# Performance work log

Measured on AMD Instinct MI355X. Metric: run time of the kernel, lower is better.

The kernel has to match this reference:

```python
import jax, jax.numpy as jnp
import numpy as np

EPS = 1e-8
TOPK = 10


def setup_inputs() -> dict:
    key = jax.random.key(0)
    kz, ky = jax.random.split(key)
    B, C, T = 128, 512, 512
    Z = jax.random.normal(kz, (B, C, T), dtype=jnp.float32)
    Y = jax.random.normal(ky, (B, C, T), dtype=jnp.float32)
    return {"Z": Z, "Y": Y}


def reference(Z, Y):
    B = Z.shape[0]
    x = Z.reshape(B, -1)  # [B, D]
    y = Y.reshape(B, -1)  # [B, D]
    # cosine similarity: sim[i, j] = x[i] . y[j] / max(|x[i]| * |y[j]|, eps)
    dots = jnp.einsum("id,jd->ij", x, y)  # [B, B]
    xn = jnp.linalg.norm(x, axis=1)  # [B]
    yn = jnp.linalg.norm(y, axis=1)  # [B]
    sim = dots / jnp.maximum(xn[:, None] * yn[None, :], EPS)
    sim = sim.T  # rows now indexed by Y, cols by Z (as in original)
    diags = jnp.arange(B)
    top1accuracy = jnp.mean((jnp.argmax(sim, axis=1) == diags).astype(jnp.float32))
    _, topk_idx = jax.lax.top_k(sim, TOPK)  # [B, 10]
    top10accuracy = jnp.mean(jnp.any(topk_idx == diags[:, None], axis=1).astype(jnp.float32))
    return (top1accuracy, top10accuracy)
```

## Files before the change

### kernel.cpp

```cpp
#include <hip/hip_runtime.h>
#include <hip/hip_bf16.h>
#include <math.h>


#define DIMD 262144

typedef short  bf16x8  __attribute__((ext_vector_type(8)));
typedef float  floatx4 __attribute__((ext_vector_type(4)));

union FragU { uint4 u; bf16x8 v; };

__global__ __launch_bounds__(512, 4)
void mfma_dot_kernel(const float* __restrict__ Z, const float* __restrict__ Y,
                     float* __restrict__ partials, float* __restrict__ norms,
                     int NT) {
    __shared__ __align__(16) ushort planes[4][128][40];

    const int tid = threadIdx.x;
    const int lid = tid & 63;
    const int w   = tid >> 6;

    const int srow = tid >> 3;
    const int q    = tid & 7;

    const int m0 = 64 * (w >> 2);
    const int n0 = 32 * (w & 3);
    const int fr = lid & 15;
    const int fk = (lid >> 4) * 8;

    floatx4 acc[4][2];
#pragma unroll
    for (int a = 0; a < 4; ++a)
#pragma unroll
        for (int b = 0; b < 2; ++b)
            acc[a][b] = (floatx4){0.f, 0.f, 0.f, 0.f};

    float z2[2] = {0.f, 0.f}, y2[2] = {0.f, 0.f};

    const uint kbase = (uint)blockIdx.x * (uint)(NT * 32);
    const uint off0  = (uint)srow * (uint)DIMD + kbase + 4u * (uint)q;
    const uint off1  = off0 + 64u * (uint)DIMD;

    float4 za[2], ya[2], zb[2], yb[2];
    za[0] = *(const float4*)(Z + off0);      za[1] = *(const float4*)(Z + off1);
    ya[0] = *(const float4*)(Y + off0);      ya[1] = *(const float4*)(Y + off1);
    zb[0] = *(const float4*)(Z + off0 + 32); zb[1] = *(const float4*)(Z + off1 + 32);
    yb[0] = *(const float4*)(Y + off0 + 32); yb[1] = *(const float4*)(Y + off1 + 32);

    auto convstore = [&](const float4 (&zr)[2], const float4 (&yr)[2]) {
#pragma unroll
        for (int i = 0; i < 2; ++i) {
            const int row = srow + 64 * i;
            {
                const float4 v = zr[i];
                const uint h0 = __float_as_uint(v.x) >> 16, h1 = __float_as_uint(v.y) >> 16;
                const uint h2 = __float_as_uint(v.z) >> 16, h3 = __float_as_uint(v.w) >> 16;
                const uint l0 = __float_as_uint(v.x - __uint_as_float(h0 << 16)) >> 16;
                const uint l1 = __float_as_uint(v.y - __uint_as_float(h1 << 16)) >> 16;
                const uint l2 = __float_as_uint(v.z - __uint_as_float(h2 << 16)) >> 16;
                const uint l3 = __float_as_uint(v.w - __uint_as_float(h3 << 16)) >> 16;
                *(uint2*)&planes[0][row][4 * q] =
                    make_uint2(h0 | (h1 << 16), h2 | (h3 << 16));
                *(uint2*)&planes[1][row][4 * q] =
                    make_uint2(l0 | (l1 << 16), l2 | (l3 << 16));
                z2[i] += v.x * v.x + v.y * v.y + v.z * v.z + v.w * v.w;
            }
            {
                const float4 v = yr[i];
                const uint h0 = __float_as_uint(v.x) >> 16, h1 = __float_as_uint(v.y) >> 16;
                const uint h2 = __float_as_uint(v.z) >> 16, h3 = __float_as_uint(v.w) >> 16;
                const uint l0 = __float_as_uint(v.x - __uint_as_float(h0 << 16)) >> 16;
                const uint l1 = __float_as_uint(v.y - __uint_as_float(h1 << 16)) >> 16;
                const uint l2 = __float_as_uint(v.z - __uint_as_float(h2 << 16)) >> 16;
                const uint l3 = __float_as_uint(v.w - __uint_as_float(h3 << 16)) >> 16;
                *(uint2*)&planes[2][row][4 * q] =
                    make_uint2(h0 | (h1 << 16), h2 | (h3 << 16));
                *(uint2*)&planes[3][row][4 * q] =
                    make_uint2(l0 | (l1 << 16), l2 | (l3 << 16));
                y2[i] += v.x * v.x + v.y * v.y + v.z * v.z + v.w * v.w;
            }
        }
    };

    auto mfma_phase = [&]() {
        FragU bh[2], bl[2];
#pragma unroll
        for (int tn = 0; tn < 2; ++tn) {
            bh[tn].u = *(const uint4*)&planes[2][n0 + 16 * tn + fr][fk];
            bl[tn].u = *(const uint4*)&planes[3][n0 + 16 * tn + fr][fk];
        }
#pragma unroll
        for (int tm = 0; tm < 4; ++tm) {
            FragU ah, al;
            ah.u = *(const uint4*)&planes[0][m0 + 16 * tm + fr][fk];
            al.u = *(const uint4*)&planes[1][m0 + 16 * tm + fr][fk];
#pragma unroll
            for (int tn = 0; tn < 2; ++tn) {
                acc[tm][tn] = __builtin_amdgcn_mfma_f32_16x16x32_bf16(ah.v, bh[tn].v, acc[tm][tn], 0, 0, 0);
                acc[tm][tn] = __builtin_amdgcn_mfma_f32_16x16x32_bf16(ah.v, bl[tn].v, acc[tm][tn], 0, 0, 0);
                acc[tm][tn] = __builtin_amdgcn_mfma_f32_16x16x32_bf16(al.v, bh[tn].v, acc[tm][tn], 0, 0, 0);
            }
        }
    };

#pragma unroll 1
    for (int t = 0; t < NT; t += 2) {
        __syncthreads();
        convstore(za, ya);
        if (t + 2 < NT) {
            const uint ko = (uint)(t + 2) * 32u;
            za[0] = *(const float4*)(Z + off0 + ko); za[1] = *(const float4*)(Z + off1 + ko);
            ya[0] = *(const float4*)(Y + off0 + ko); ya[1] = *(const float4*)(Y + off1 + ko);
        }
        __syncthreads();
        mfma_phase();

        __syncthreads();
        convstore(zb, yb);
        if (t + 3 < NT) {
            const uint ko = (uint)(t + 3) * 32u;
            zb[0] = *(const float4*)(Z + off0 + ko); zb[1] = *(const float4*)(Z + off1 + ko);
            yb[0] = *(const float4*)(Y + off0 + ko); yb[1] = *(const float4*)(Y + off1 + ko);
        }
        __syncthreads();
        mfma_phase();
    }

#pragma unroll
    for (int m = 1; m <= 4; m <<= 1) {
        z2[0] += __shfl_xor(z2[0], m); z2[1] += __shfl_xor(z2[1], m);
        y2[0] += __shfl_xor(y2[0], m); y2[1] += __shfl_xor(y2[1], m);
    }
    if (q == 0) {
        atomicAdd(&norms[srow],            z2[0]);
        atomicAdd(&norms[srow + 64],       z2[1]);
        atomicAdd(&norms[128 + srow],      y2[0]);
        atomicAdd(&norms[128 + srow + 64], y2[1]);
    }

    float* P = partials + (size_t)blockIdx.x * 16384;
    const int rq = (lid >> 4) * 4;
#pragma unroll
    for (int tm = 0; tm < 4; ++tm)
#pragma unroll
        for (int tn = 0; tn < 2; ++tn)
#pragma unroll
            for (int r = 0; r < 4; ++r)
                P[(size_t)(m0 + 16 * tm + rq + r) * 128 + (n0 + 16 * tn + fr)] =
                    acc[tm][tn][r];
}

#define BK   16
#define LSTR 132
__global__ __launch_bounds__(256)
void dot_norm_atomic(const float* __restrict__ Z, const float* __restrict__ Y,
                     float* __restrict__ dots, float* __restrict__ norms,
                     int KC) {
    __shared__ float lA[BK][LSTR];
    __shared__ float lB[BK][LSTR];
    const int tid = threadIdx.x;
    const int tx = tid & 15, ty = tid >> 4;
    const int r0 = ty * 8, c0 = tx * 8;
    const int rowm = tid >> 2, kq = tid & 3;
    float acc[8][8];
#pragma unroll
    for (int i = 0; i < 8; ++i)
#pragma unroll
        for (int j = 0; j < 8; ++j) acc[i][j] = 0.f;
    float a2s0 = 0.f, a2s1 = 0.f, b2s0 = 0.f, b2s1 = 0.f;
    const size_t kbase = (size_t)blockIdx.x * KC;
    const size_t offA0 = (size_t)rowm * DIMD + kbase + kq * 4;
    const size_t offA1 = (size_t)(rowm + 64) * DIMD + kbase + kq * 4;
    const int niter = KC / BK;
#pragma unroll 1
    for (int t = 0; t < niter; ++t) {
        const size_t ko = (size_t)t * BK;
        const float4 av0 = *(const float4*)(Z + offA0 + ko);
        const float4 av1 = *(const float4*)(Z + offA1 + ko);
        const float4 bv0 = *(const float4*)(Y + offA0 + ko);
        const float4 bv1 = *(const float4*)(Y + offA1 + ko);
        a2s0 += av0.x*av0.x + av0.y*av0.y + av0.z*av0.z + av0.w*av0.w;
        a2s1 += av1.x*av1.x + av1.y*av1.y + av1.z*av1.z + av1.w*av1.w;
        b2s0 += bv0.x*bv0.x + bv0.y*bv0.y + bv0.z*bv0.z + bv0.w*bv0.w;
        b2s1 += bv1.x*bv1.x + bv1.y*bv1.y + bv1.z*bv1.z + bv1.w*bv1.w;
        __syncthreads();
        const int kk = kq * 4;
        lA[kk+0][rowm]    = av0.x; lA[kk+1][rowm]    = av0.y;
        lA[kk+2][rowm]    = av0.z; lA[kk+3][rowm]    = av0.w;
        lA[kk+0][rowm+64] = av1.x; lA[kk+1][rowm+64] = av1.y;
        lA[kk+2][rowm+64] = av1.z; lA[kk+3][rowm+64] = av1.w;
        lB[kk+0][rowm]    = bv0.x; lB[kk+1][rowm]    = bv0.y;
        lB[kk+2][rowm]    = bv0.z; lB[kk+3][rowm]    = bv0.w;
        lB[kk+0][rowm+64] = bv1.x; lB[kk+1][rowm+64] = bv1.y;
        lB[kk+2][rowm+64] = bv1.z; lB[kk+3][rowm+64] = bv1.w;
        __syncthreads();
#pragma unroll
        for (int k = 0; k < BK; ++k) {
            const float4 a0 = *(const float4*)&lA[k][r0];
            const float4 a1 = *(const float4*)&lA[k][r0 + 4];
            const float4 b0 = *(const float4*)&lB[k][c0];
            const float4 b1 = *(const float4*)&lB[k][c0 + 4];
            const float a[8] = {a0.x,a0.y,a0.z,a0.w,a1.x,a1.y,a1.z,a1.w};
            const float b[8] = {b0.x,b0.y,b0.z,b0.w,b1.x,b1.y,b1.z,b1.w};
#pragma unroll
            for (int i = 0; i < 8; ++i)
#pragma unroll
                for (int j = 0; j < 8; ++j)
                    acc[i][j] = fmaf(a[i], b[j], acc[i][j]);
        }
    }
    __syncthreads();
    float* nrm = &lA[0][0];
    nrm[tid] = 0.f;
    __syncthreads();
    atomicAdd(&nrm[rowm],            a2s0);
    atomicAdd(&nrm[rowm + 64],       a2s1);
    atomicAdd(&nrm[128 + rowm],      b2s0);
    atomicAdd(&nrm[128 + rowm + 64], b2s1);
    __syncthreads();
    atomicAdd(&norms[tid], nrm[tid]);
#pragma unroll
    for (int i = 0; i < 8; ++i)
#pragma unroll
        for (int j = 0; j < 8; ++j)
            atomicAdd(&dots[(size_t)(r0 + i) * 128 + (c0 + j)], acc[i][j]);
}

__global__ __launch_bounds__(256)
void reduce_stage1(const float* __restrict__ partials, float* __restrict__ stage,
                   int per_chunk) {
    const int g = blockIdx.x * 256 + threadIdx.x;
    const int f4 = g & 4095;
    const int chunk = g >> 12;
    const float4* p = (const float4*)partials;
    float4 s = make_float4(0.f, 0.f, 0.f, 0.f);
    const size_t base = (size_t)chunk * per_chunk;
    for (int k = 0; k < per_chunk; ++k) {
        const float4 v = p[(base + k) * 4096 + f4];
        s.x += v.x; s.y += v.y; s.z += v.z; s.w += v.w;
    }
    ((float4*)stage)[(size_t)chunk * 4096 + f4] = s;
}

__global__ __launch_bounds__(128)
void rank_kernel(const float* __restrict__ stage, const float* __restrict__ norms,
                 float* __restrict__ out, int nchunks) {
    __shared__ float sim[128];
    __shared__ int cnt;
    const int a = blockIdx.x;
    const int b = threadIdx.x;
    float s = 0.f;
    for (int c = 0; c < nchunks; ++c)
        s += stage[(size_t)c * 16384 + (size_t)b * 128 + a];
    const float v = s / fmaxf(sqrtf(norms[b]) * sqrtf(norms[128 + a]), 1e-8f);
    sim[b] = v;
    if (b == 0) cnt = 0;
    __syncthreads();
    const float diag = sim[a];
    if (b != a && v > diag) atomicAdd(&cnt, 1);
    __syncthreads();
    if (b == 0) {
        if (cnt == 0) atomicAdd(&out[0], 1.0f / 128.0f);
        if (cnt < 10) atomicAdd(&out[1], 1.0f / 128.0f);
    }
}

extern "C" void kernel_launch(void* const* d_in, const int* in_sizes, int n_in,
                              void* d_out, int out_size, void* d_ws, size_t ws_size,
                              hipStream_t stream) {
    const float* Z = (const float*)d_in[0];
    const float* Y = (const float*)d_in[1];
    float* dots     = (float*)d_ws;
    float* norms    = dots + 128 * 128;
    float* stage    = norms + 256;
    float* partials = stage + 32 * 16384;
    float* out      = (float*)d_out;

    const size_t head_floats = 128 * 128 + 256 + 32 * 16384;
    int nb = 0;
    const int cands[2] = {512, 256};
    for (int c = 0; c < 2; ++c) {
        if ((head_floats + (size_t)cands[c] * 16384) * sizeof(float) <= ws_size) {
            nb = cands[c];
            break;
        }
    }

    hipMemsetAsync(d_ws, 0, (128 * 128 + 256) * sizeof(float), stream);
    hipMemsetAsync(d_out, 0, 2 * sizeof(float), stream);

    if (nb > 0) {
        mfma_dot_kernel<<<nb, 512, 0, stream>>>(Z, Y, partials, norms,
                                                DIMD / nb / 32);
        reduce_stage1<<<512, 256, 0, stream>>>(partials, stage, nb / 32);
        rank_kernel<<<128, 128, 0, stream>>>(stage, norms, out, 32);
    } else {
        dot_norm_atomic<<<512, 256, 0, stream>>>(Z, Y, dots, norms, DIMD / 512);
        rank_kernel<<<128, 128, 0, stream>>>(dots, norms, out, 1);
    }
}
```

Baseline: 317.9 us.

## Stage fp32 tiles via direct global-to-LDS loads, convert to bf16 hi/lo at fragment load

Replaces register-staged loads plus conversion and store into bf16 planes with asynchronous global_load_lds copies of raw fp32 tiles into a double-buffered, XOR-swizzled LDS layout. The hi/lo bf16 split now happens per fragment when reading from LDS, and the squared norms are computed from the LDS tile. This removes one barrier per step and the VGPR round-trip, letting the next tile load overlap the MFMA work. The cost is doubled LDS footprint, which may lower occupancy, and redundant conversion work, since each fragment row is converted by several waves.

```diff
diff --git a/kernel.cpp b/kernel.cpp
--- a/kernel.cpp
+++ b/kernel.cpp
@@ -9,24 +9,47 @@
 typedef float  floatx4 __attribute__((ext_vector_type(4)));
 
 union FragU { uint4 u; bf16x8 v; };
+
+#define GLOAD_LDS16(g, l)                                        \
+    __builtin_amdgcn_global_load_lds(                            \
+        (const __attribute__((address_space(1))) void*)(g),      \
+        (__attribute__((address_space(3))) void*)(l), 16, 0, 0)
+
+static __device__ __forceinline__ void cvt_hilo(const float4 f0, const float4 f1,
+                                                bf16x8& hv, bf16x8& lv) {
+    const float ff[8] = {f0.x, f0.y, f0.z, f0.w, f1.x, f1.y, f1.z, f1.w};
+    uint hu[4], lu[4];
+#pragma unroll
+    for (int j = 0; j < 4; ++j) {
+        const uint b0  = __float_as_uint(ff[2 * j]);
+        const uint b1  = __float_as_uint(ff[2 * j + 1]);
+        const uint hf0 = b0 & 0xffff0000u;
+        const uint hf1 = b1 & 0xffff0000u;
+        hu[j] = (b0 >> 16) | hf1;
+        const uint lo0 = __float_as_uint(ff[2 * j]     - __uint_as_float(hf0));
+        const uint lo1 = __float_as_uint(ff[2 * j + 1] - __uint_as_float(hf1));
+        lu[j] = (lo0 >> 16) | (lo1 & 0xffff0000u);
+    }
+    FragU h, l;
+    h.u = make_uint4(hu[0], hu[1], hu[2], hu[3]);
+    l.u = make_uint4(lu[0], lu[1], lu[2], lu[3]);
+    hv = h.v; lv = l.v;
+}
 
 __global__ __launch_bounds__(512, 4)
 void mfma_dot_kernel(const float* __restrict__ Z, const float* __restrict__ Y,
                      float* __restrict__ partials, float* __restrict__ norms,
                      int NT) {
-    __shared__ __align__(16) ushort planes[4][128][40];
+    __shared__ __align__(16) float ldsf[2][2][128][32];
 
     const int tid = threadIdx.x;
     const int lid = tid & 63;
     const int w   = tid >> 6;
 
-    const int srow = tid >> 3;
-    const int q    = tid & 7;
-
-    const int m0 = 64 * (w >> 2);
-    const int n0 = 32 * (w & 3);
-    const int fr = lid & 15;
-    const int fk = (lid >> 4) * 8;
+    const int m0  = 64 * (w >> 2);
+    const int n0  = 32 * (w & 3);
+    const int fr  = lid & 15;
+    const int fkc = (lid >> 4) * 2;
 
     floatx4 acc[4][2];
 #pragma unroll
@@ -35,108 +58,75 @@
         for (int b = 0; b < 2; ++b)
             acc[a][b] = (floatx4){0.f, 0.f, 0.f, 0.f};
 
-    float z2[2] = {0.f, 0.f}, y2[2] = {0.f, 0.f};
-
-    const uint kbase = (uint)blockIdx.x * (uint)(NT * 32);
-    const uint off0  = (uint)srow * (uint)DIMD + kbase + 4u * (uint)q;
-    const uint off1  = off0 + 64u * (uint)DIMD;
-
-    float4 za[2], ya[2], zb[2], yb[2];
-    za[0] = *(const float4*)(Z + off0);      za[1] = *(const float4*)(Z + off1);
-    ya[0] = *(const float4*)(Y + off0);      ya[1] = *(const float4*)(Y + off1);
-    zb[0] = *(const float4*)(Z + off0 + 32); zb[1] = *(const float4*)(Z + off1 + 32);
-    yb[0] = *(const float4*)(Y + off0 + 32); yb[1] = *(const float4*)(Y + off1 + 32);
-
-    auto convstore = [&](const float4 (&zr)[2], const float4 (&yr)[2]) {
-#pragma unroll
-        for (int i = 0; i < 2; ++i) {
-            const int row = srow + 64 * i;
-            {
-                const float4 v = zr[i];
-                const uint h0 = __float_as_uint(v.x) >> 16, h1 = __float_as_uint(v.y) >> 16;
-                const uint h2 = __float_as_uint(v.z) >> 16, h3 = __float_as_uint(v.w) >> 16;
-                const uint l0 = __float_as_uint(v.x - __uint_as_float(h0 << 16)) >> 16;
-                const uint l1 = __float_as_uint(v.y - __uint_as_float(h1 << 16)) >> 16;
-                const uint l2 = __float_as_uint(v.z - __uint_as_float(h2 << 16)) >> 16;
-                const uint l3 = __float_as_uint(v.w - __uint_as_float(h3 << 16)) >> 16;
-                *(uint2*)&planes[0][row][4 * q] =
-                    make_uint2(h0 | (h1 << 16), h2 | (h3 << 16));
-                *(uint2*)&planes[1][row][4 * q] =
-                    make_uint2(l0 | (l1 << 16), l2 | (l3 << 16));
-                z2[i] += v.x * v.x + v.y * v.y + v.z * v.z + v.w * v.w;
+    const size_t kbase = (size_t)blockIdx.x * ((size_t)NT * 32);
+    const int    w16   = 16 * w;
+    const int    csrc  = ((lid & 7) ^ (lid >> 3)) * 4;
+    const size_t g0    = (size_t)(w16 + (lid >> 3)) * DIMD + kbase + csrc;
+    const size_t g1    = g0 + 8ull * DIMD;
+
+    auto stage = [&](int b, size_t ko) {
+        GLOAD_LDS16(Z + g0 + ko, &ldsf[b][0][w16][0]);
+        GLOAD_LDS16(Z + g1 + ko, &ldsf[b][0][w16 + 8][0]);
+        GLOAD_LDS16(Y + g0 + ko, &ldsf[b][1][w16][0]);
+        GLOAD_LDS16(Y + g1 + ko, &ldsf[b][1][w16 + 8][0]);
+    };
+
+    const int nmat = tid >> 8;
+    const int nrow = (tid >> 1) & 127;
+    const int nh4  = (tid & 1) * 4;
+    const int nsw  = nrow & 7;
+    float nsum = 0.f;
+
+    stage(0, 0);
+    __syncthreads();
+
+#pragma unroll 1
+    for (int t = 0; t < NT; ++t) {
+        const int b = t & 1;
+        if (t + 1 < NT) stage(b ^ 1, (size_t)(t + 1) * 32);
+
+        FragU dummy;
+        bf16x8 bh[2], bl[2];
+#pragma unroll
+        for (int tn = 0; tn < 2; ++tn) {
+            const int r = n0 + 16 * tn + fr;
+            const int s = r & 7;
+            const float* rp = &ldsf[b][1][r][0];
+            const float4 f0 = *(const float4*)(rp + ((fkc ^ s) * 4));
+            const float4 f1 = *(const float4*)(rp + (((fkc + 1) ^ s) * 4));
+            cvt_hilo(f0, f1, bh[tn], bl[tn]);
+        }
+#pragma unroll
+        for (int tm = 0; tm < 4; ++tm) {
+            const int r = m0 + 16 * tm + fr;
+            const int s = r & 7;
+            const float* rp = &ldsf[b][0][r][0];
+            const float4 f0 = *(const float4*)(rp + ((fkc ^ s) * 4));
+            const float4 f1 = *(const float4*)(rp + (((fkc + 1) ^ s) * 4));
+            bf16x8 ah, al;
+            cvt_hilo(f0, f1, ah, al);
+#pragma unroll
+            for (int tn = 0; tn < 2; ++tn) {
+                acc[tm][tn] = __builtin_amdgcn_mfma_f32_16x16x32_bf16(ah, bh[tn], acc[tm][tn], 0, 0, 0);
+                acc[tm][tn] = __builtin_amdgcn_mfma_f32_16x16x32_bf16(ah, bl[tn], acc[tm][tn], 0, 0, 0);
+                acc[tm][tn] = __builtin_amdgcn_mfma_f32_16x16x32_bf16(al, bh[tn], acc[tm][tn], 0, 0, 0);
             }
-            {
-                const float4 v = yr[i];
-                const uint h0 = __float_as_uint(v.x) >> 16, h1 = __float_as_uint(v.y) >> 16;
-                const uint h2 = __float_as_uint(v.z) >> 16, h3 = __float_as_uint(v.w) >> 16;
-                const uint l0 = __float_as_uint(v.x - __uint_as_float(h0 << 16)) >> 16;
-                const uint l1 = __float_as_uint(v.y - __uint_as_float(h1 << 16)) >> 16;
-                const uint l2 = __float_as_uint(v.z - __uint_as_float(h2 << 16)) >> 16;
-                const uint l3 = __float_as_uint(v.w - __uint_as_float(h3 << 16)) >> 16;
-                *(uint2*)&planes[2][row][4 * q] =
-                    make_uint2(h0 | (h1 << 16), h2 | (h3 << 16));
-                *(uint2*)&planes[3][row][4 * q] =
-                    make_uint2(l0 | (l1 << 16), l2 | (l3 << 16));
-                y2[i] += v.x * v.x + v.y * v.y + v.z * v.z + v.w * v.w;
+        }
+
+        {
+            const float* rp = &ldsf[b][nmat][nrow][0];
+#pragma unroll
+            for (int j = 0; j < 4; ++j) {
+                const float4 v = *(const float4*)(rp + (((nh4 + j) ^ nsw) * 4));
+                nsum += v.x * v.x + v.y * v.y + v.z * v.z + v.w * v.w;
             }
         }
-    };
-
-    auto mfma_phase = [&]() {
-        FragU bh[2], bl[2];
-#pragma unroll
-        for (int tn = 0; tn < 2; ++tn) {
-            bh[tn].u = *(const uint4*)&planes[2][n0 + 16 * tn + fr][fk];
-            bl[tn].u = *(const uint4*)&planes[3][n0 + 16 * tn + fr][fk];
-        }
-#pragma unroll
-        for (int tm = 0; tm < 4; ++tm) {
-            FragU ah, al;
-            ah.u = *(const uint4*)&planes[0][m0 + 16 * tm + fr][fk];
-            al.u = *(const uint4*)&planes[1][m0 + 16 * tm + fr][fk];
-#pragma unroll
-            for (int tn = 0; tn < 2; ++tn) {
-                acc[tm][tn] = __builtin_amdgcn_mfma_f32_16x16x32_bf16(ah.v, bh[tn].v, acc[tm][tn], 0, 0, 0);
-                acc[tm][tn] = __builtin_amdgcn_mfma_f32_16x16x32_bf16(ah.v, bl[tn].v, acc[tm][tn], 0, 0, 0);
-                acc[tm][tn] = __builtin_amdgcn_mfma_f32_16x16x32_bf16(al.v, bh[tn].v, acc[tm][tn], 0, 0, 0);
-            }
-        }
-    };
-
-#pragma unroll 1
-    for (int t = 0; t < NT; t += 2) {
+
         __syncthreads();
-        convstore(za, ya);
-        if (t + 2 < NT) {
-            const uint ko = (uint)(t + 2) * 32u;
-            za[0] = *(const float4*)(Z + off0 + ko); za[1] = *(const float4*)(Z + off1 + ko);
-            ya[0] = *(const float4*)(Y + off0 + ko); ya[1] = *(const float4*)(Y + off1 + ko);
-        }
-        __syncthreads();
-        mfma_phase();
-
-        __syncthreads();
-        convstore(zb, yb);
-        if (t + 3 < NT) {
-            const uint ko = (uint)(t + 3) * 32u;
-            zb[0] = *(const float4*)(Z + off0 + ko); zb[1] = *(const float4*)(Z + off1 + ko);
-            yb[0] = *(const float4*)(Y + off0 + ko); yb[1] = *(const float4*)(Y + off1 + ko);
-        }
-        __syncthreads();
-        mfma_phase();
-    }
-
-#pragma unroll
-    for (int m = 1; m <= 4; m <<= 1) {
-        z2[0] += __shfl_xor(z2[0], m); z2[1] += __shfl_xor(z2[1], m);
-        y2[0] += __shfl_xor(y2[0], m); y2[1] += __shfl_xor(y2[1], m);
-    }
-    if (q == 0) {
-        atomicAdd(&norms[srow],            z2[0]);
-        atomicAdd(&norms[srow + 64],       z2[1]);
-        atomicAdd(&norms[128 + srow],      y2[0]);
-        atomicAdd(&norms[128 + srow + 64], y2[1]);
-    }
+    }
+
+    nsum += __shfl_xor(nsum, 1);
+    if ((tid & 1) == 0) atomicAdd(&norms[nmat * 128 + nrow], nsum);
 
     float* P = partials + (size_t)blockIdx.x * 16384;
     const int rq = (lid >> 4) * 4;
```

Result: no change. 313.1 us (-1.5%).
